# Performance work log

Measured on AMD Instinct MI355X. Metric: run time of the kernel, lower is better.

## Reference

```python
import jax, jax.numpy as jnp
import numpy as np

PATCH = 3
PAD = 1  # (patchsize-1)//2
PRETRAIN_DIM = 1024
TARGET_DIM = 1024
OUT_H, OUT_W = 224, 224


def _pool_matrix(L_in, L_out):
    """Matrix P s.t. x @ P == torch.adaptive_avg_pool1d(x, L_out)."""
    P = np.zeros((L_in, L_out), dtype=np.float32)
    for i in range(L_out):
        s = (i * L_in) // L_out
        e = -((-(i + 1) * L_in) // L_out)  # ceil
        P[s:e, i] = 1.0 / (e - s)
    return jnp.asarray(P)


def patchify(x):
    """[B,C,H,W] -> [B,H*W,C,3,3], matching Unfold(k=3,s=1,p=1) + reshape/permute."""
    B, C, H, W = x.shape
    xp = jnp.pad(x, ((0, 0), (0, 0), (PAD, PAD), (PAD, PAD)))
    # [B,C,3,3,H,W] with kernel offsets (ki,kj)
    cols = jnp.stack([
        jnp.stack([xp[:, :, i:i + H, j:j + W] for j in range(PATCH)], axis=3)
        for i in range(PATCH)], axis=2)
    return cols.transpose(0, 4, 5, 1, 2, 3).reshape(B, H * W, C, PATCH, PATCH)


def resize_bilinear(x, oh, ow):
    """Bilinear resize of last two dims, align_corners=False (torch semantics)."""
    H, W = x.shape[-2], x.shape[-1]

    def idx(L, O):
        src = (jnp.arange(O, dtype=jnp.float32) + 0.5) * (L / O) - 0.5
        src = jnp.clip(src, 0.0, L - 1)
        i0 = jnp.floor(src).astype(jnp.int32)
        i1 = jnp.minimum(i0 + 1, L - 1)
        return i0, i1, src - i0

    r0, r1, wr = idx(H, oh)
    c0, c1, wc = idx(W, ow)
    xr = x[..., r0, :] * (1.0 - wr)[:, None] + x[..., r1, :] * wr[:, None]
    return xr[..., c0] * (1.0 - wc) + xr[..., c1] * wc


def setup_inputs() -> dict:
    key = jax.random.key(0)
    k1, k2, k3 = jax.random.split(key, 3)
    return {
        "feat1": jax.random.normal(k1, (8, 512, 28, 28), dtype=jnp.float32),
        "feat2": jax.random.normal(k2, (8, 1024, 14, 14), dtype=jnp.float32),
        "memory": jax.random.normal(k3, (20000, 1024), dtype=jnp.float32),
    }


def reference(feat1, feat2, memory):
    B, C1, H1, W1 = feat1.shape
    _, C2, H2, W2 = feat2.shape
    N = H1 * W1  # reference patch grid

    # --- patchify (Unfold k=3 s=1 p=1) ---
    p1 = patchify(feat1)                      # [B, N, C1, 3, 3]
    p2 = patchify(feat2)                      # [B, H2*W2, C2, 3, 3]

    # --- multiscale bilinear resize of layer-2 patch grid to ref grid ---
    g = p2.reshape(B, H2, W2, C2, PATCH, PATCH).transpose(0, 3, 4, 5, 1, 2)  # [B,C2,3,3,H2,W2]
    g = resize_bilinear(g, H1, W1)                                           # [B,C2,3,3,H1,W1]
    p2 = g.transpose(0, 4, 5, 1, 2, 3).reshape(B, N, C2, PATCH, PATCH)

    # --- Preprocessing: adaptive_avg_pool1d over flattened patch -> pretrain dim ---
    f1 = p1.reshape(B * N, C1 * PATCH * PATCH) @ _pool_matrix(C1 * PATCH * PATCH, PRETRAIN_DIM)
    f2 = p2.reshape(B * N, C2 * PATCH * PATCH) @ _pool_matrix(C2 * PATCH * PATCH, PRETRAIN_DIM)

    # --- Aggregator: stack layers, adaptive pool to target dim ---
    stacked = jnp.stack([f1, f2], axis=1).reshape(B * N, 2 * PRETRAIN_DIM)
    feats = stacked @ _pool_matrix(2 * PRETRAIN_DIM, TARGET_DIM)  # [B*N, D]

    # --- kNN memory-bank scoring (k=1): min Euclidean distance ---
    d2 = (jnp.sum(feats * feats, axis=-1, keepdims=True)
          - 2.0 * feats @ memory.T
          + jnp.sum(memory * memory, axis=-1))  # [B*N, M]
    dist = jnp.sqrt(jnp.maximum(d2, 0.0))
    patch_scores = jnp.min(dist, axis=1)       # [B*N]

    # --- unpatch + score + raw segmentation map ---
    ps = patch_scores.reshape(B, N)
    image_scores = jnp.max(ps, axis=1)                           # [B]
    raw_maps = resize_bilinear(ps.reshape(B, H1, W1), OUT_H, OUT_W)  # [B,224,224]
    return image_scores, raw_maps
```

## Files before the change

### kernel.cpp

```cpp
#include <hip/hip_runtime.h>
#include <hip/hip_bf16.h>
#include <math.h>

#define BQ 8
#define C1N 512
#define N1 784
#define C2N 1024
#define M2 196
#define NROWS 6272
#define MEMN 20000
#define MEMNP 20096
#define DIMK 1024
#define NKB 32
#define AKB 4096
#define BKB 4096
#define OUTHW 50176
#define NTILEA 49
#define NTILEB 157
#define NWG (NTILEB * NTILEA)

typedef unsigned char u8;
typedef long long i64;
typedef __attribute__((ext_vector_type(2))) long long ll2;
typedef __attribute__((ext_vector_type(4))) float f32x4;

static __device__ __forceinline__ unsigned int f2ord(float f) {
  unsigned int b = __float_as_uint(f);
  return (b & 0x80000000u) ? ~b : (b | 0x80000000u);
}
static __device__ __forceinline__ float ord2f(unsigned int u) {
  unsigned int b = (u & 0x80000000u) ? (u ^ 0x80000000u) : ~u;
  return __uint_as_float(b);
}

static __device__ __forceinline__ int pack4_fp8(float a, float b, float c, float d) {
  int lo = __builtin_amdgcn_cvt_pk_fp8_f32(a, b, 0, false);
  return __builtin_amdgcn_cvt_pk_fp8_f32(c, d, lo, true);
}
static __device__ __forceinline__ float sumsq4_fp8(int w) {
  float f0 = __builtin_amdgcn_cvt_f32_fp8(w, 0);
  float f1 = __builtin_amdgcn_cvt_f32_fp8(w, 1);
  float f2 = __builtin_amdgcn_cvt_f32_fp8(w, 2);
  float f3 = __builtin_amdgcn_cvt_f32_fp8(w, 3);
  return f0 * f0 + f1 * f1 + f2 * f2 + f3 * f3;
}

static __device__ __forceinline__ void gload16(const void* g, void* l) {
  __builtin_amdgcn_global_load_lds((const __attribute__((address_space(1))) void*)g,
                                   (__attribute__((address_space(3))) void*)l, 16, 0, 0);
}

static __device__ __forceinline__ size_t tiled_a_idx(int grow, int k) {
  int tile = grow >> 7, row = grow & 127;
  int half = row >> 6, mi = (row >> 4) & 3, frow = row & 15;
  int kb = k >> 5, fc = (k >> 3) & 3, e = k & 7;
  return ((((((size_t)(tile * NKB + kb) * 2 + half) * 4 + fc) * 16 + frow) * 4 + mi) << 3) + e;
}

static __device__ __forceinline__ float f1val(const float* __restrict__ x, int b, unsigned L) {
  unsigned h = L % 28u; unsigned t = L / 28u;
  unsigned ki = t % 3u; t /= 3u;
  unsigned c = t % 512u; t /= 512u;
  unsigned w = t % 28u; unsigned kj = t / 28u;
  unsigned y = h + ki - 1u;
  unsigned xx = w + kj - 1u;
  if (y >= 28u || xx >= 28u) return 0.f;
  return x[(((size_t)b * 512u + c) * 28u + y) * 28u + xx];
}
static __device__ __forceinline__ float f2val(const float* __restrict__ x, int b, unsigned L) {
  unsigned h = L % 14u; unsigned t = L / 14u;
  unsigned ki = t % 3u; t /= 3u;
  unsigned c = t % 1024u; t /= 1024u;
  unsigned w = t % 14u; unsigned kj = t / 14u;
  unsigned y = h + ki - 1u;
  unsigned xx = w + kj - 1u;
  if (y >= 14u || xx >= 14u) return 0.f;
  return x[(((size_t)b * 1024u + c) * 14u + y) * 14u + xx];
}

__global__ __launch_bounds__(256) void feat_a_fp8(const float* __restrict__ feat1,
                                                  u8* __restrict__ At) {
  int id = blockIdx.x * 256 + threadIdx.x;
  if (id >= BQ * N1 * 512) return;
  int j = id & 511; int t = id >> 9;
  int n = t % N1; int b = t / N1;
  unsigned L0 = 9u * (unsigned)(512 * n + j);
  float s = 0.f;
#pragma unroll
  for (int u = 0; u < 9; ++u) s += f1val(feat1, b, L0 + u);
  s += f1val(feat1, b, L0 + 4u);
  int p = __builtin_amdgcn_cvt_pk_fp8_f32(s * 0.1f, s * 0.1f, 0, false);
  At[tiled_a_idx(b * N1 + n, j)] = (u8)(p & 0xFF);
}

__global__ __launch_bounds__(256) void feat_b_stage1(const float* __restrict__ feat2,
                                                     float* __restrict__ H2all) {
  int b = blockIdx.x / M2;
  int n2 = blockIdx.x % M2;
  for (int i = threadIdx.x; i < 512; i += 256) {
    unsigned L0 = 18u * (unsigned)(512 * n2 + i);
    float s = 0.f;
#pragma unroll
    for (int u = 0; u < 18; ++u) s += f2val(feat2, b, L0 + u);
    H2all[((size_t)b * M2 + n2) * 512 + i] = s * (1.0f / 18.0f);
  }
}

__global__ __launch_bounds__(256) void feat_b_stage2_fp8(const float* __restrict__ H2all,
                                                         u8* __restrict__ At) {
  int id = blockIdx.x * 256 + threadIdx.x;
  if (id >= BQ * 64 * N1) return;
  int n = id % N1; int t = id / N1;
  int ic = t % 64; int b = t / 64;
  int y = n / 28, x = n % 28;
  float sy = 0.5f * (float)y - 0.25f;
  sy = fminf(fmaxf(sy, 0.f), 13.f);
  int y0 = (int)sy, y1 = min(y0 + 1, 13);
  float wy = sy - (float)y0;
  float sx = 0.5f * (float)x - 0.25f;
  sx = fminf(fmaxf(sx, 0.f), 13.f);
  int x0 = (int)sx, x1 = min(x0 + 1, 13);
  float wx = sx - (float)x0;
  float w00 = (1.f - wy) * (1.f - wx), w10 = wy * (1.f - wx);
  float w01 = (1.f - wy) * wx, w11 = wy * wx;
  const float* h00 = H2all + ((size_t)b * M2 + y0 * 14 + x0) * 512 + ic * 8;
  const float* h10 = H2all + ((size_t)b * M2 + y1 * 14 + x0) * 512 + ic * 8;
  const float* h01 = H2all + ((size_t)b * M2 + y0 * 14 + x1) * 512 + ic * 8;
  const float* h11 = H2all + ((size_t)b * M2 + y1 * 14 + x1) * 512 + ic * 8;
  float v[8];
#pragma unroll
  for (int e = 0; e < 8; ++e)
    v[e] = w00 * h00[e] + w10 * h10[e] + w01 * h01[e] + w11 * h11[e];
  int w0 = pack4_fp8(v[0], v[1], v[2], v[3]);
  int w1 = pack4_fp8(v[4], v[5], v[6], v[7]);
  *(int2*)&At[tiled_a_idx(b * N1 + n, 512 + ic * 8)] = make_int2(w0, w1);
}

__global__ __launch_bounds__(256) void memconv_fp8(const float* __restrict__ mem,
                                                   u8* __restrict__ Bt) {
  int gid = blockIdx.x * 256 + threadIdx.x;
  if (gid >= NTILEB * NKB * 512) return;
  int tile = gid >> 14;
  int within = gid & 16383;
  int kb = within >> 9;
  int u = within & 511;
  int c = u >> 7, row = u & 127;
  int n = tile * 128 + row;
  int k0 = kb * 32 + c * 8;
  int w0 = 0, w1 = 0;
  if (n < MEMN) {
    const float* src = mem + (size_t)n * DIMK + k0;
    float4 a = *(const float4*)src;
    float4 b = *(const float4*)(src + 4);
    w0 = pack4_fp8(a.x, a.y, a.z, a.w);
    w1 = pack4_fp8(b.x, b.y, b.z, b.w);
  }
  *(int2*)&Bt[(size_t)gid * 8] = make_int2(w0, w1);
}

__global__ __launch_bounds__(256) void mnorm_fp8(const u8* __restrict__ Bt,
                                                 float* __restrict__ mnorm) {
  __shared__ float part[2][128];
  int tile = blockIdx.x;
  int r = threadIdx.x & 127, hh = threadIdx.x >> 7;
  const u8* base = Bt + (size_t)tile * (NKB * BKB) + r * 8;
  float s = 0.f;
#pragma unroll 4
  for (int ch = hh * 64; ch < hh * 64 + 64; ++ch) {
    int2 d = *(const int2*)(base + (size_t)ch * 1024);
    s += sumsq4_fp8(d.x) + sumsq4_fp8(d.y);
  }
  part[hh][r] = s;
  __syncthreads();
  if (threadIdx.x < 128) {
    int n = tile * 128 + threadIdx.x;
    if (n < MEMN) mnorm[n] = part[0][threadIdx.x] + part[1][threadIdx.x];
  }
}

__global__ __launch_bounds__(256, 4) void dist_min_mfma(const u8* __restrict__ At,
                                                        const u8* __restrict__ Bt,
                                                        const float* __restrict__ mnorm,
                                                        unsigned int* __restrict__ minu) {
  __shared__ __align__(16) u8 LBs[4][4096];
  const int t = threadIdx.x;
  const int wave = t >> 6, lane = t & 63;

  int lid = blockIdx.x;
  const int q = NWG / 8, r = NWG % 8;
  int xcd = lid & 7, pos = lid >> 3;
  int wgid = (xcd < r ? xcd * (q + 1) : r * (q + 1) + (xcd - r) * q) + pos;
  int g = wgid / (NTILEB * 7), rem = wgid % (NTILEB * 7);
  int bx = rem / 7;
  int by = g * 7 + rem % 7;
  const int row0 = by * 128, col0 = bx * 128;

  f32x4 acc[4][4];
#pragma unroll
  for (int i = 0; i < 4; ++i)
#pragma unroll
    for (int j = 0; j < 4; ++j) acc[i][j] = (f32x4){0.f, 0.f, 0.f, 0.f};

  const int wr = (wave >> 1) * 64, wc = (wave & 1) * 64;
  const int frow = lane & 15, fc = lane >> 4;
  const int half = wave >> 1;
  const int boff = fc * 1024 + (wc + frow) * 8;

  const u8* aP = At + (size_t)by * (NKB * AKB) + ((half * 4 + fc) * 16 + frow) * 32;
  const u8* bG = Bt + (size_t)bx * (NKB * BKB) + t * 16;

  ll2 ar0[2], ar1[2];

#define LOAD_A(P, kb)                                        \
  do {                                                       \
    const u8* p_ = aP + (size_t)(kb) * AKB;                  \
    ar##P[0] = *(const ll2*)p_;                              \
    ar##P[1] = *(const ll2*)(p_ + 16);                       \
  } while (0)

#define STAGE_B(S, kb) gload16(bG + (size_t)(kb) * BKB, &LBs[S][wave * 1024])

#define SBAR __builtin_amdgcn_s_barrier()
#define VMW(n) asm volatile("s_waitcnt vmcnt(" #n ")" ::: "memory")

#define COMPUTE(S, P)                                                                        \
  do {                                                                                       \
    i64 b[4];                                                                                \
    _Pragma("unroll") for (int ni = 0; ni < 4; ++ni)                                         \
        b[ni] = *(const i64*)&LBs[S][boff + ni * 128];                                       \
    i64 a0_ = ar##P[0].x, a1_ = ar##P[0].y, a2_ = ar##P[1].x, a3_ = ar##P[1].y;              \
    __builtin_amdgcn_s_setprio(1);                                                           \
    _Pragma("unroll") for (int ni = 0; ni < 4; ++ni) {                                       \
      acc[0][ni] = __builtin_amdgcn_mfma_f32_16x16x32_fp8_fp8(a0_, b[ni], acc[0][ni], 0, 0, 0); \
      acc[1][ni] = __builtin_amdgcn_mfma_f32_16x16x32_fp8_fp8(a1_, b[ni], acc[1][ni], 0, 0, 0); \
      acc[2][ni] = __builtin_amdgcn_mfma_f32_16x16x32_fp8_fp8(a2_, b[ni], acc[2][ni], 0, 0, 0); \
      acc[3][ni] = __builtin_amdgcn_mfma_f32_16x16x32_fp8_fp8(a3_, b[ni], acc[3][ni], 0, 0, 0); \
    }                                                                                        \
    __builtin_amdgcn_s_setprio(0);                                                           \
  } while (0)

#define ITER(S, P, PN, kA, kS)       \
  do {                               \
    LOAD_A(PN, kA);                  \
    STAGE_B((S + 3) & 3, kS);        \
    COMPUTE(S, P);                   \
    VMW(6);                          \
    SBAR;                            \
  } while (0)

  LOAD_A(0, 0);
  STAGE_B(0, 0);
  STAGE_B(1, 1);
  STAGE_B(2, 2);
  VMW(0);
  SBAR;

#pragma unroll 1
  for (int i = 0; i < 7; ++i) {
    int k = i * 4;
    ITER(0, 0, 1, k + 1, k + 3);
    ITER(1, 1, 0, k + 2, k + 4);
    ITER(2, 0, 1, k + 3, k + 5);
    ITER(3, 1, 0, k + 4, k + 6);
  }
  LOAD_A(1, 29); STAGE_B(3, 31); COMPUTE(0, 0); VMW(6); SBAR;
  LOAD_A(0, 30); COMPUTE(1, 1); VMW(5); SBAR;
  LOAD_A(1, 31); COMPUTE(2, 0); VMW(4); SBAR;
  COMPUTE(3, 1);
#undef ITER
#undef COMPUTE
#undef LOAD_A
#undef STAGE_B
#undef VMW

  float cmn[4];
#pragma unroll
  for (int ni = 0; ni < 4; ++ni) {
    int gn = col0 + wc + ni * 16 + frow;
    cmn[ni] = (gn < MEMN) ? mnorm[gn] : INFINITY;
  }
#pragma unroll
  for (int mi = 0; mi < 4; ++mi) {
#pragma unroll
    for (int rr = 0; rr < 4; ++rr) {
      float v = INFINITY;
#pragma unroll
      for (int ni = 0; ni < 4; ++ni)
        v = fminf(v, fmaf(-2.f, acc[mi][ni][rr], cmn[ni]));
#pragma unroll
      for (int off = 1; off < 16; off <<= 1)
        v = fminf(v, __shfl_xor(v, off, 64));
      if (frow == 0) {
        int grow = row0 + wr + mi * 16 + fc * 4 + rr;
        atomicMin(&minu[grow], f2ord(v));
      }
    }
  }
}


__global__ __launch_bounds__(256) void scores_fused(const u8* __restrict__ At,
                                                    const unsigned int* __restrict__ minu,
                                                    float* __restrict__ scores) {
  int row = blockIdx.x * 4 + (threadIdx.x >> 6);
  int lane = threadIdx.x & 63;
  float s = 0.f;
#pragma unroll
  for (int qq = 0; qq < 2; ++qq) {
    int2 d = *(const int2*)&At[tiled_a_idx(row, (lane + qq * 64) * 8)];
    s += sumsq4_fp8(d.x);
    s += sumsq4_fp8(d.y);
  }
#pragma unroll
  for (int off = 32; off; off >>= 1) s += __shfl_down(s, off, 64);
  if (lane == 0) scores[row] = sqrtf(fmaxf(s + ord2f(minu[row]), 0.f));
}

__global__ __launch_bounds__(256) void image_max_kernel(const float* __restrict__ scores,
                                                        float* __restrict__ out) {
  __shared__ float red[4];
  const int b = blockIdx.x;
  float m = -INFINITY;
  for (int n = threadIdx.x; n < N1; n += 256) m = fmaxf(m, scores[b * N1 + n]);
#pragma unroll
  for (int off = 32; off; off >>= 1) m = fmaxf(m, __shfl_down(m, off, 64));
  if ((threadIdx.x & 63) == 0) red[threadIdx.x >> 6] = m;
  __syncthreads();
  if (threadIdx.x == 0) out[b] = fmaxf(fmaxf(red[0], red[1]), fmaxf(red[2], red[3]));
}

__global__ __launch_bounds__(256) void upsample_kernel(const float* __restrict__ scores,
                                                       float* __restrict__ out) {
  int o = blockIdx.x * 256 + threadIdx.x;
  if (o >= BQ * OUTHW) return;
  int b = o / OUTHW, rem = o % OUTHW;
  int oy = rem / 224, ox = rem % 224;
  float sy = ((float)oy + 0.5f) * 0.125f - 0.5f;
  sy = fminf(fmaxf(sy, 0.f), 27.f);
  int y0 = (int)sy, y1 = min(y0 + 1, 27);
  float wy = sy - (float)y0;
  float sx = ((float)ox + 0.5f) * 0.125f - 0.5f;
  sx = fminf(fmaxf(sx, 0.f), 27.f);
  int x0 = (int)sx, x1 = min(x0 + 1, 27);
  float wx = sx - (float)x0;
  const float* s = scores + b * N1;
  float v0 = s[y0 * 28 + x0] * (1.f - wy) + s[y1 * 28 + x0] * wy;
  float v1 = s[y0 * 28 + x1] * (1.f - wy) + s[y1 * 28 + x1] * wy;
  out[BQ + o] = v0 * (1.f - wx) + v1 * wx;
}

extern "C" void kernel_launch(void* const* d_in, const int* in_sizes, int n_in,
                              void* d_out, int out_size, void* d_ws, size_t ws_size,
                              hipStream_t stream) {
  const float* feat1 = (const float*)d_in[0];
  const float* feat2 = (const float*)d_in[1];
  const float* memory = (const float*)d_in[2];
  float* out = (float*)d_out;

  char* ws = (char*)d_ws;
  size_t off = 0;
  auto wsalloc = [&](size_t bytes) {
    void* p = ws + off;
    off += (bytes + 255) & ~(size_t)255;
    return p;
  };

  u8* At = (u8*)wsalloc((size_t)NTILEA * NKB * AKB);
  u8* Bt = (u8*)wsalloc((size_t)NTILEB * NKB * BKB);
  float* mnorm = (float*)wsalloc((size_t)MEMN * 4);
  unsigned int* minu = (unsigned int*)wsalloc((size_t)NROWS * 4);
  float* scores = (float*)wsalloc((size_t)NROWS * 4);
  float* H2all = (float*)Bt;

  feat_a_fp8<<<(BQ * N1 * 512) / 256, 256, 0, stream>>>(feat1, At);
  feat_b_stage1<<<BQ * M2, 256, 0, stream>>>(feat2, H2all);
  feat_b_stage2_fp8<<<(BQ * 64 * N1) / 256, 256, 0, stream>>>(H2all, At);
  memconv_fp8<<<(NTILEB * NKB * 512) / 256, 256, 0, stream>>>(memory, Bt);
  mnorm_fp8<<<NTILEB, 256, 0, stream>>>(Bt, mnorm);
  (void)hipMemsetAsync(minu, 0xFF, (size_t)NROWS * 4, stream);

  dist_min_mfma<<<NWG, 256, 0, stream>>>(At, Bt, mnorm, minu);

  scores_fused<<<NROWS / 4, 256, 0, stream>>>(At, minu, scores);
  image_max_kernel<<<BQ, 256, 0, stream>>>(scores, out);
  upsample_kernel<<<(BQ * OUTHW + 255) / 256, 256, 0, stream>>>(scores, out);
}
```

Baseline: 303.7 us.

## Switch FP8 distance GEMM to 32x32x16 MFMA with matching A layout

Replaces the 16x16x32 FP8 MFMA tiling with 32x32x16 instructions, giving each wave 2x2 accumulators of 16 floats instead of 4x4 of 4. The pre-tiled A layout, the B LDS read offsets and the epilogue row mapping and shuffle reduction are all reworked to match the new operand and output layouts. The larger MFMA shape needs fewer instructions and fewer LDS B reads per k-step and may use the matrix units more efficiently. In exchange the cross-lane min reduction gains an extra shuffle stage and correctness depends on the new index mapping being exact.

```diff
diff --git a/kernel.cpp b/kernel.cpp
--- a/kernel.cpp
+++ b/kernel.cpp
@@ -22,7 +22,7 @@
 typedef unsigned char u8;
 typedef long long i64;
 typedef __attribute__((ext_vector_type(2))) long long ll2;
-typedef __attribute__((ext_vector_type(4))) float f32x4;
+typedef __attribute__((ext_vector_type(16))) float f32x16;
 
 static __device__ __forceinline__ unsigned int f2ord(float f) {
   unsigned int b = __float_as_uint(f);
@@ -51,10 +51,10 @@
 }
 
 static __device__ __forceinline__ size_t tiled_a_idx(int grow, int k) {
-  int tile = grow >> 7, row = grow & 127;
-  int half = row >> 6, mi = (row >> 4) & 3, frow = row & 15;
-  int kb = k >> 5, fc = (k >> 3) & 3, e = k & 7;
-  return ((((((size_t)(tile * NKB + kb) * 2 + half) * 4 + fc) * 16 + frow) * 4 + mi) << 3) + e;
+  int tile = grow >> 7, rowt = grow & 127;
+  int wrb = rowt >> 6, mi = (rowt >> 5) & 1, r = rowt & 31;
+  int kb = k >> 5, kh = (k >> 4) & 1, kg = (k >> 3) & 1, e = k & 7;
+  return ((((size_t)(tile * NKB + kb) * 2 + wrb) * 2 + kg) * 32 + r) * 32 + mi * 16 + kh * 8 + e;
 }
 
 static __device__ __forceinline__ float f1val(const float* __restrict__ x, int b, unsigned L) {
@@ -195,18 +195,18 @@
   int by = g * 7 + rem % 7;
   const int row0 = by * 128, col0 = bx * 128;
 
-  f32x4 acc[4][4];
-#pragma unroll
-  for (int i = 0; i < 4; ++i)
-#pragma unroll
-    for (int j = 0; j < 4; ++j) acc[i][j] = (f32x4){0.f, 0.f, 0.f, 0.f};
-
-  const int wr = (wave >> 1) * 64, wc = (wave & 1) * 64;
-  const int frow = lane & 15, fc = lane >> 4;
-  const int half = wave >> 1;
-  const int boff = fc * 1024 + (wc + frow) * 8;
-
-  const u8* aP = At + (size_t)by * (NKB * AKB) + ((half * 4 + fc) * 16 + frow) * 32;
+  f32x16 acc[2][2];
+#pragma unroll
+  for (int i = 0; i < 2; ++i)
+#pragma unroll
+    for (int j = 0; j < 2; ++j) acc[i][j] = (f32x16)0.0f;
+
+  const int wrb = wave >> 1;
+  const int wr = wrb * 64, wc = (wave & 1) * 64;
+  const int kg = lane >> 5, r32 = lane & 31;
+  const int boff = kg * 1024 + (wc + r32) * 8;
+
+  const u8* aP = At + (size_t)by * (NKB * AKB) + ((wrb * 2 + kg) * 32 + r32) * 32;
   const u8* bG = Bt + (size_t)bx * (NKB * BKB) + t * 16;
 
   ll2 ar0[2], ar1[2];
@@ -225,17 +225,19 @@
 
 #define COMPUTE(S, P)                                                                        \
   do {                                                                                       \
-    i64 b[4];                                                                                \
-    _Pragma("unroll") for (int ni = 0; ni < 4; ++ni)                                         \
-        b[ni] = *(const i64*)&LBs[S][boff + ni * 128];                                       \
-    i64 a0_ = ar##P[0].x, a1_ = ar##P[0].y, a2_ = ar##P[1].x, a3_ = ar##P[1].y;              \
+    i64 b00 = *(const i64*)&LBs[S][boff];                                                    \
+    i64 b01 = *(const i64*)&LBs[S][boff + 256];                                              \
+    i64 b10 = *(const i64*)&LBs[S][boff + 2048];                                             \
+    i64 b11 = *(const i64*)&LBs[S][boff + 2304];                                             \
     __builtin_amdgcn_s_setprio(1);                                                           \
-    _Pragma("unroll") for (int ni = 0; ni < 4; ++ni) {                                       \
-      acc[0][ni] = __builtin_amdgcn_mfma_f32_16x16x32_fp8_fp8(a0_, b[ni], acc[0][ni], 0, 0, 0); \
-      acc[1][ni] = __builtin_amdgcn_mfma_f32_16x16x32_fp8_fp8(a1_, b[ni], acc[1][ni], 0, 0, 0); \
-      acc[2][ni] = __builtin_amdgcn_mfma_f32_16x16x32_fp8_fp8(a2_, b[ni], acc[2][ni], 0, 0, 0); \
-      acc[3][ni] = __builtin_amdgcn_mfma_f32_16x16x32_fp8_fp8(a3_, b[ni], acc[3][ni], 0, 0, 0); \
-    }                                                                                        \
+    acc[0][0] = __builtin_amdgcn_mfma_f32_32x32x16_fp8_fp8(ar##P[0].x, b00, acc[0][0], 0, 0, 0); \
+    acc[1][0] = __builtin_amdgcn_mfma_f32_32x32x16_fp8_fp8(ar##P[1].x, b00, acc[1][0], 0, 0, 0); \
+    acc[0][1] = __builtin_amdgcn_mfma_f32_32x32x16_fp8_fp8(ar##P[0].x, b01, acc[0][1], 0, 0, 0); \
+    acc[1][1] = __builtin_amdgcn_mfma_f32_32x32x16_fp8_fp8(ar##P[1].x, b01, acc[1][1], 0, 0, 0); \
+    acc[0][0] = __builtin_amdgcn_mfma_f32_32x32x16_fp8_fp8(ar##P[0].y, b10, acc[0][0], 0, 0, 0); \
+    acc[1][0] = __builtin_amdgcn_mfma_f32_32x32x16_fp8_fp8(ar##P[1].y, b10, acc[1][0], 0, 0, 0); \
+    acc[0][1] = __builtin_amdgcn_mfma_f32_32x32x16_fp8_fp8(ar##P[0].y, b11, acc[0][1], 0, 0, 0); \
+    acc[1][1] = __builtin_amdgcn_mfma_f32_32x32x16_fp8_fp8(ar##P[1].y, b11, acc[1][1], 0, 0, 0); \
     __builtin_amdgcn_s_setprio(0);                                                           \
   } while (0)
 
@@ -273,25 +275,23 @@
 #undef STAGE_B
 #undef VMW
 
-  float cmn[4];
-#pragma unroll
-  for (int ni = 0; ni < 4; ++ni) {
-    int gn = col0 + wc + ni * 16 + frow;
+  float cmn[2];
+#pragma unroll
+  for (int ni = 0; ni < 2; ++ni) {
+    int gn = col0 + wc + ni * 32 + r32;
     cmn[ni] = (gn < MEMN) ? mnorm[gn] : INFINITY;
   }
 #pragma unroll
-  for (int mi = 0; mi < 4; ++mi) {
-#pragma unroll
-    for (int rr = 0; rr < 4; ++rr) {
-      float v = INFINITY;
-#pragma unroll
-      for (int ni = 0; ni < 4; ++ni)
-        v = fminf(v, fmaf(-2.f, acc[mi][ni][rr], cmn[ni]));
-#pragma unroll
-      for (int off = 1; off < 16; off <<= 1)
+  for (int mi = 0; mi < 2; ++mi) {
+#pragma unroll
+    for (int reg = 0; reg < 16; ++reg) {
+      float v = fminf(fmaf(-2.f, acc[mi][0][reg], cmn[0]),
+                      fmaf(-2.f, acc[mi][1][reg], cmn[1]));
+#pragma unroll
+      for (int off = 1; off < 32; off <<= 1)
         v = fminf(v, __shfl_xor(v, off, 64));
-      if (frow == 0) {
-        int grow = row0 + wr + mi * 16 + fc * 4 + rr;
+      if (r32 == 0) {
+        int grow = row0 + wr + mi * 32 + (reg & 3) + 8 * (reg >> 2) + 4 * kg;
         atomicMin(&minu[grow], f2ord(v));
       }
     }
```

Result: slower. 368.3 us (+21.3%).
